# Kernel tuning notes

Hardware: AMD Instinct MI355X
Metric: run time of the kernel (lower is better)

## Reference

```python
import jax, jax.numpy as jnp
import numpy as np

J = 17        # number of joints (hard-coded in module)
H = 32        # h_dim
DIM = 2       # 2D keypoint input dim
N_TRUE = 9    # visible joints per sample (constant count required by reshape)
N_FALSE = J - N_TRUE
SLOPE = 0.01  # LeakyReLU default negative slope


def leaky(x):
    return jax.nn.leaky_relu(x, SLOPE)


def setup_inputs() -> dict:
    key = jax.random.key(0)
    ks = jax.random.split(key, 16)
    B = 65536
    x = jax.random.normal(ks[0], (B, J, DIM), jnp.float32)
    # mask with exactly N_TRUE True entries per row (random positions)
    perm = jnp.argsort(jax.random.uniform(ks[1], (B, J)), axis=1)
    m = jnp.zeros((B, J), bool).at[jnp.arange(B)[:, None], perm[:, :N_TRUE]].set(True)

    def lin(k, i, o):
        k1, k2 = jax.random.split(k)
        s = 1.0 / np.sqrt(i)
        # weights stored (in, out) so forward is x @ W + b
        return (jax.random.uniform(k1, (i, o), jnp.float32, -s, s),
                jax.random.uniform(k2, (o,), jnp.float32, -s, s))

    W_up, b_up = lin(ks[2], DIM * J, H * J)        # ScoreMechain.up_dim
    positions = jax.random.normal(ks[3], (1, J, H), jnp.float32)
    W_ud, b_ud = lin(ks[4], H + H, H)              # SelfAtt.up_dim (dim=h_dim=32)
    W_q, b_q = lin(ks[5], H, H)
    W_k, b_k = lin(ks[6], H, H)
    W_v, b_v = lin(ks[7], H, H)
    W_d1, b_d1 = lin(ks[8], H, H)                  # SelfAtt.down_dim[0]
    W_d2, b_d2 = lin(ks[9], H, H)                  # SelfAtt.down_dim[2]
    W_s, b_s = lin(ks[10], H, 1)                   # ScoreMechain.down_dim
    return dict(x=x, m=m, positions=positions, W_up=W_up, b_up=b_up,
                W_ud=W_ud, b_ud=b_ud, W_q=W_q, b_q=b_q, W_k=W_k, b_k=b_k,
                W_v=W_v, b_v=b_v, W_d1=W_d1, b_d1=b_d1, W_d2=W_d2, b_d2=b_d2,
                W_s=W_s, b_s=b_s)


def reference(x, m, positions, W_up, b_up, W_ud, b_ud, W_q, b_q, W_k, b_k,
              W_v, b_v, W_d1, b_d1, W_d2, b_d2, W_s, b_s):
    B = x.shape[0]
    # ScoreMechain: flatten joints, lift to (B, 17, H)
    up = leaky(x.reshape(B, -1) @ W_up + b_up).reshape(B, J, H)
    # static-count mask split via stable argsort (True-indices first / False-indices first)
    idx_t = jnp.argsort(~m, axis=1, stable=True)[:, :N_TRUE]   # visible joints
    idx_f = jnp.argsort(m, axis=1, stable=True)[:, :N_FALSE]   # occluded joints
    take = lambda a, i: jnp.take_along_axis(a, i[:, :, None], axis=1)
    x1 = take(up, idx_t)                       # (B, 9, H)
    x2 = take(up, idx_f)                       # (B, 8, H)
    # SelfAtt
    p = jnp.broadcast_to(positions, (B, J, H))
    kpos = take(p, idx_t)
    qpos = take(p, idx_f)
    x1c = jnp.concatenate([x1, kpos], axis=-1)  # (B, 9, 2H)
    x2c = jnp.concatenate([x2, qpos], axis=-1)  # (B, 8, 2H)
    u1 = leaky(x1c @ W_ud + b_ud)
    u2 = leaky(x2c @ W_ud + b_ud)
    ux = jnp.concatenate([u1, u2], axis=1)      # (B, 17, H)
    q = u2 @ W_q + b_q                          # (B, 8, H)
    k = ux @ W_k + b_k                          # (B, 17, H)
    v = ux @ W_v + b_v
    # SelfAtt was built as SelfAtt(h_dim) => scale = sqrt(32)
    att = jax.nn.softmax(jnp.einsum('bqh,bkh->bqk', q, k) / jnp.sqrt(jnp.float32(H)), axis=-1)
    o = jnp.einsum('bqk,bkh->bqh', att, v)      # (B, 8, H)
    o = (leaky(o @ W_d1 + b_d1) @ W_d2 + b_d2) + x2  # residual = x2c[..., :H] = x2
    return jax.nn.sigmoid(o @ W_s + b_s)[..., 0]     # (B, 8)
```

## Files before the change

### kernel.cpp

```cpp
#include <hip/hip_runtime.h>
#include <hip/hip_fp16.h>

#define JN 17

typedef __fp16 h2v __attribute__((ext_vector_type(2)));
typedef _Float16 f16x8 __attribute__((ext_vector_type(8)));
typedef float f32x4 __attribute__((ext_vector_type(4)));

__device__ __forceinline__ float lrelu(float x){ return fmaxf(x, 0.01f*x); }
__device__ __forceinline__ unsigned h2u(h2v h){ unsigned u; __builtin_memcpy(&u, &h, 4); return u; }
__device__ __forceinline__ h2v u2h(unsigned u){ h2v h; __builtin_memcpy(&h, &u, 4); return h; }
__device__ __forceinline__ unsigned pkrtz(float a, float b){ return h2u(__builtin_amdgcn_cvt_pkrtz(a,b)); }
__device__ __forceinline__ float fdot2(unsigned a, unsigned b, float c){
    return __builtin_amdgcn_fdot2(u2h(a), u2h(b), c, false);
}
__device__ __forceinline__ unsigned pkfma(unsigned a, unsigned b, unsigned c){
    h2v r = u2h(a)*u2h(b) + u2h(c);
    return h2u(r);
}
__device__ __forceinline__ f16x8 u4h8(uint4 u){ union{uint4 u; f16x8 h;} c; c.u=u; return c.h; }
__device__ __forceinline__ f32x4 mk4(float4 v){ f32x4 r; r[0]=v.x; r[1]=v.y; r[2]=v.z; r[3]=v.w; return r; }

__device__ __forceinline__ f16x8 repack(f32x4 c0, f32x4 c1, int srcA, int srcB, bool selLo){
    unsigned pkA = pkrtz(c0[0], c0[1]);
    unsigned pkB = pkrtz(c0[2], c0[3]);
    unsigned pkC = pkrtz(c1[0], c1[1]);
    unsigned pkD = pkrtz(c1[2], c1[3]);
    unsigned rA0 = (unsigned)__shfl((int)pkA, srcA, 64);
    unsigned rB0 = (unsigned)__shfl((int)pkB, srcA, 64);
    unsigned rC0 = (unsigned)__shfl((int)pkC, srcA, 64);
    unsigned rD0 = (unsigned)__shfl((int)pkD, srcA, 64);
    unsigned rA1 = (unsigned)__shfl((int)pkA, srcB, 64);
    unsigned rB1 = (unsigned)__shfl((int)pkB, srcB, 64);
    unsigned rC1 = (unsigned)__shfl((int)pkC, srcB, 64);
    unsigned rD1 = (unsigned)__shfl((int)pkD, srcB, 64);
    uint4 u;
    u.x = selLo ? rA0 : rC0;
    u.y = selLo ? rB0 : rD0;
    u.z = selLo ? rA1 : rC1;
    u.w = selLo ? rB1 : rD1;
    return u4h8(u);
}

#define OFF_PP    0
#define OFF_BQS   544
#define OFF_FQ    576
#define OFF_FD1   1088
#define OFF_FD2   1600
#define OFF_FUD   2112
#define OFF_FK    2624
#define OFF_FV    3136
#define OFF_TUP   3648
#define OFF_FUP   4192
#define HDR_BYTES 65536

#define KSTRIDE 276
#define QSTRIDE 132

__global__ __launch_bounds__(256,1)
void prep_kernel(const void* __restrict__ mraw, const float* __restrict__ pos,
                 const float* __restrict__ Wup,
                 const float* __restrict__ Wud, const float* __restrict__ bud,
                 const float* __restrict__ Wq,  const float* __restrict__ bq,
                 const float* __restrict__ Wk,  const float* __restrict__ Wv,
                 const float* __restrict__ Wd1, const float* __restrict__ Wd2,
                 unsigned* __restrict__ ws32, unsigned* __restrict__ bmask, int B)
{
    int g = blockIdx.x*256 + threadIdx.x;
    const float isq = 0.17677669529663687f;

    const unsigned* mw = (const unsigned*)mraw;
    bool f3f=false, nz=false;
    #pragma unroll
    for (int i=0;i<17;i++){
        unsigned w = mw[i];
        if ((w>>24) == 0x3Fu) f3f = true;
        if (w & 0xFFFFFF00u)  nz  = true;
    }
    int mode = f3f ? 2 : (nz ? 1 : 0);
    if (g < B){
        unsigned bm = 0; size_t base = (size_t)g*JN;
        if (mode == 0){
            const int* mi = (const int*)mraw;
            #pragma unroll
            for (int j=0;j<JN;j++) if (mi[base+j] != 0) bm |= (1u<<j);
        } else if (mode == 1){
            const unsigned char* mb = (const unsigned char*)mraw;
            #pragma unroll
            for (int j=0;j<JN;j++) if (mb[base+j] != 0) bm |= (1u<<j);
        } else {
            const float* mf = (const float*)mraw;
            #pragma unroll
            for (int j=0;j<JN;j++) if (mf[base+j] != 0.f) bm |= (1u<<j);
        }
        bmask[g] = bm;
    }
    if (g < 544){
        int j = g >> 5, h = g & 31;
        float acc = bud[h];
        #pragma unroll
        for (int c=0;c<32;c++) acc = fmaf(pos[j*32+c], Wud[(32+c)*32 + h], acc);
        ((float*)ws32)[OFF_PP + g] = acc;
        int t = (g >> 4) & 1, c = g & 15;
        int col = j*32 + t*16 + c;
        ws32[OFF_TUP + g] = pkrtz(Wup[32*544 + col], Wup[33*544 + col]);
    }
    if (g < 32) ((float*)ws32)[OFF_BQS + g] = bq[g]*isq;
    if (g < 512){
        int t = g >> 8, rmn = g & 255, lane = rmn >> 2, i2 = rmn & 3;
        int k0 = (lane>>4)*8 + 2*i2, c = (lane&15) + 16*t;
        ws32[OFF_FUD + g] = pkrtz(Wud[k0*32 + c],     Wud[(k0+1)*32 + c]);
        ws32[OFF_FK  + g] = pkrtz(Wk [k0*32 + c],     Wk [(k0+1)*32 + c]);
        ws32[OFF_FV  + g] = pkrtz(Wv [k0*32 + c],     Wv [(k0+1)*32 + c]);
        ws32[OFF_FQ  + g] = pkrtz(Wq [k0*32 + c]*isq, Wq [(k0+1)*32 + c]*isq);
        ws32[OFF_FD1 + g] = pkrtz(Wd1[(k0>>1)*32 + c], Wd1[(16 + (k0>>1))*32 + c]);
        ws32[OFF_FD2 + g] = pkrtz(Wd2[k0*32 + c],     Wd2[(k0+1)*32 + c]);
    }
    if (g < 8704){
        int j = g >> 9, r = g & 511, t = r >> 8, rr = r & 255, lane = rr >> 2, i2 = rr & 3;
        int k0 = (lane>>4)*8 + 2*i2;
        int col = j*32 + (lane&15) + 16*t;
        ws32[OFF_FUP + g] = pkrtz(Wup[k0*544 + col], Wup[(k0+1)*544 + col]);
    }
}

__global__ __launch_bounds__(256,3)
void fused_kernel(const float* __restrict__ x, const unsigned* __restrict__ bmask,
                  const unsigned* __restrict__ ws32,
                  const float* __restrict__ bup, const float* __restrict__ bk,
                  const float* __restrict__ bv,  const float* __restrict__ bd1,
                  const float* __restrict__ bd2, const float* __restrict__ Ws,
                  const float* __restrict__ bs,  float* __restrict__ out, int B)
{
    __shared__ unsigned ksl[16*KSTRIDE];
    __shared__ unsigned vsl[16*KSTRIDE];
    __shared__ unsigned qsl[16*QSTRIDE];
    __shared__ unsigned usl[16*QSTRIDE];

    const int tid = threadIdx.x;
    const int wid = tid >> 6, wl = tid & 63;
    const int sb  = blockIdx.x * 16;
    const int s   = wl & 15, g4 = wl >> 4;
    const int smax = B - 1;

    {
        int sA = sb + s; if (sA > smax) sA = smax;
        f16x8 ax;
        {
            const float* xr = x + (size_t)sA*34 + g4*8;
            float2 a0 = *(const float2*)(xr);
            float2 a1 = *(const float2*)(xr+2);
            float2 a2 = *(const float2*)(xr+4);
            float2 a3 = *(const float2*)(xr+6);
            uint4 u; u.x=pkrtz(a0.x,a0.y); u.y=pkrtz(a1.x,a1.y);
            u.z=pkrtz(a2.x,a2.y); u.w=pkrtz(a3.x,a3.y);
            ax = u4h8(u);
        }
        const unsigned bm = bmask[sA];
        float2 xt2 = *(const float2*)(x + (size_t)sA*34 + 32);
        const unsigned xtp = pkrtz(xt2.x, xt2.y);

        const uint4* wsu4 = (const uint4*)ws32;
        f16x8 fud0 = u4h8(wsu4[OFF_FUD/4 + wl]);
        f16x8 fud1 = u4h8(wsu4[OFF_FUD/4 + 64 + wl]);
        f16x8 fk0  = u4h8(wsu4[OFF_FK/4  + wl]);
        f16x8 fk1  = u4h8(wsu4[OFF_FK/4  + 64 + wl]);
        f16x8 fv0  = u4h8(wsu4[OFF_FV/4  + wl]);
        f16x8 fv1  = u4h8(wsu4[OFF_FV/4  + 64 + wl]);
        f16x8 fq0  = u4h8(wsu4[OFF_FQ/4  + wl]);
        f16x8 fq1  = u4h8(wsu4[OFF_FQ/4  + 64 + wl]);

        const float* ppf = (const float*)ws32;
        float4 bk0 = *(const float4*)(bk + g4*4);
        float4 bk1 = *(const float4*)(bk + 16 + g4*4);
        float4 bv0 = *(const float4*)(bv + g4*4);
        float4 bv1 = *(const float4*)(bv + 16 + g4*4);
        float4 bq0 = *(const float4*)(ppf + OFF_BQS + g4*4);
        float4 bq1 = *(const float4*)(ppf + OFF_BQS + 16 + g4*4);

        const int srcA = s + 32*(g4 & 1);
        const int srcB = srcA + 16;
        const bool selLo = (g4 < 2);

        const int njl = (wid == 3) ? 5 : 4;
        for (int jj = 0; jj < njl; jj++){
            const int j = (jj < 4) ? (wid + jj*4) : 16;
            f16x8 fup0 = u4h8(wsu4[OFF_FUP/4 + j*128 + wl]);
            f16x8 fup1 = u4h8(wsu4[OFF_FUP/4 + j*128 + 64 + wl]);
            float4 bu0 = *(const float4*)(bup + j*32 + g4*4);
            float4 bu1 = *(const float4*)(bup + j*32 + 16 + g4*4);
            float4 pp0 = *(const float4*)(ppf + OFF_PP + j*32 + g4*4);
            float4 pp1 = *(const float4*)(ppf + OFF_PP + j*32 + 16 + g4*4);
            uint4 tu0 = *(const uint4*)(ws32 + OFF_TUP + j*32 + g4*4);
            uint4 tu1 = *(const uint4*)(ws32 + OFF_TUP + j*32 + 16 + g4*4);

            f32x4 up0, up1;
            up0[0] = fdot2(xtp, tu0.x, bu0.x); up0[1] = fdot2(xtp, tu0.y, bu0.y);
            up0[2] = fdot2(xtp, tu0.z, bu0.z); up0[3] = fdot2(xtp, tu0.w, bu0.w);
            up1[0] = fdot2(xtp, tu1.x, bu1.x); up1[1] = fdot2(xtp, tu1.y, bu1.y);
            up1[2] = fdot2(xtp, tu1.z, bu1.z); up1[3] = fdot2(xtp, tu1.w, bu1.w);
            up0 = __builtin_amdgcn_mfma_f32_16x16x32_f16(fup0, ax, up0, 0,0,0);
            up1 = __builtin_amdgcn_mfma_f32_16x16x32_f16(fup1, ax, up1, 0,0,0);
            #pragma unroll
            for (int r=0;r<4;r++){ up0[r] = lrelu(up0[r]); up1[r] = lrelu(up1[r]); }

            const bool occ = !((bm>>j)&1u);
            const int rk = __popc((~bm) & ((1u<<j)-1u));
            if (occ){
                int rotq = (rk + s + (s>>2)) & 3;
                uint4 u;
                u.x = pkrtz(up0[0], up1[0]); u.y = pkrtz(up0[1], up1[1]);
                u.z = pkrtz(up0[2], up1[2]); u.w = pkrtz(up0[3], up1[3]);
                *(uint4*)&usl[s*QSTRIDE + rk*16 + ((g4 + rotq)&3)*4] = u;
            }
            f16x8 aup = repack(up0, up1, srcA, srcB, selLo);

            f32x4 uu0 = mk4(pp0), uu1 = mk4(pp1);
            uu0 = __builtin_amdgcn_mfma_f32_16x16x32_f16(fud0, aup, uu0, 0,0,0);
            uu1 = __builtin_amdgcn_mfma_f32_16x16x32_f16(fud1, aup, uu1, 0,0,0);
            #pragma unroll
            for (int r=0;r<4;r++){ uu0[r] = lrelu(uu0[r]); uu1[r] = lrelu(uu1[r]); }
            f16x8 auu = repack(uu0, uu1, srcA, srcB, selLo);

            f32x4 kk0 = mk4(bk0), kk1 = mk4(bk1);
            f32x4 vv0 = mk4(bv0), vv1 = mk4(bv1);
            f32x4 qq0 = mk4(bq0), qq1 = mk4(bq1);
            kk0 = __builtin_amdgcn_mfma_f32_16x16x32_f16(fk0, auu, kk0, 0,0,0);
            kk1 = __builtin_amdgcn_mfma_f32_16x16x32_f16(fk1, auu, kk1, 0,0,0);
            vv0 = __builtin_amdgcn_mfma_f32_16x16x32_f16(fv0, auu, vv0, 0,0,0);
            vv1 = __builtin_amdgcn_mfma_f32_16x16x32_f16(fv1, auu, vv1, 0,0,0);
            qq0 = __builtin_amdgcn_mfma_f32_16x16x32_f16(fq0, auu, qq0, 0,0,0);
            qq1 = __builtin_amdgcn_mfma_f32_16x16x32_f16(fq1, auu, qq1, 0,0,0);

            const int rot = (j + s + (s>>2)) & 3;
            const int grp = ((g4 + rot)&3)*4;
            uint4 kp, vp;
            kp.x = pkrtz(kk0[0], kk1[0]); kp.y = pkrtz(kk0[1], kk1[1]);
            kp.z = pkrtz(kk0[2], kk1[2]); kp.w = pkrtz(kk0[3], kk1[3]);
            vp.x = pkrtz(vv0[0], vv1[0]); vp.y = pkrtz(vv0[1], vv1[1]);
            vp.z = pkrtz(vv0[2], vv1[2]); vp.w = pkrtz(vv0[3], vv1[3]);
            *(uint4*)&ksl[s*KSTRIDE + j*16 + grp] = kp;
            *(uint4*)&vsl[s*KSTRIDE + j*16 + grp] = vp;
            if (occ){
                int rotq = (rk + s + (s>>2)) & 3;
                uint4 qp4;
                qp4.x = pkrtz(qq0[0], qq1[0]); qp4.y = pkrtz(qq0[1], qq1[1]);
                qp4.z = pkrtz(qq0[2], qq1[2]); qp4.w = pkrtz(qq0[3], qq1[3]);
                *(uint4*)&qsl[s*QSTRIDE + rk*16 + ((g4 + rotq)&3)*4] = qp4;
            }
        }
    }
    __syncthreads();

    const int pr = tid;
    const int s2 = (pr >> 3) & 15, q = pr & 7;
    const bool act2 = (tid < 128) && (sb + s2 < B);
    unsigned o[16];
    #pragma unroll
    for (int p=0;p<16;p++) o[p] = 0u;
    if (act2){
        unsigned qw[16];
        {
            int rot = (q + s2 + (s2>>2)) & 3;
            const unsigned* base = qsl + s2*QSTRIDE + q*16;
            #pragma unroll
            for (int a=0;a<4;a++){
                uint4 t = *(const uint4*)(base + ((a + rot)&3)*4);
                qw[4*a]=t.x; qw[4*a+1]=t.y; qw[4*a+2]=t.z; qw[4*a+3]=t.w;
            }
        }
        float sc[JN];
        #pragma unroll
        for (int kj=0; kj<JN; kj++){
            unsigned kw[16];
            int rot = (kj + s2 + (s2>>2)) & 3;
            const unsigned* base = ksl + s2*KSTRIDE + kj*16;
            #pragma unroll
            for (int a=0;a<4;a++){
                uint4 t = *(const uint4*)(base + ((a + rot)&3)*4);
                kw[4*a]=t.x; kw[4*a+1]=t.y; kw[4*a+2]=t.z; kw[4*a+3]=t.w;
            }
            float s0=0.f,s1=0.f,s2a=0.f,s3=0.f;
            #pragma unroll
            for (int p=0;p<16;p+=4){
                s0  = fdot2(qw[p],   kw[p],   s0);
                s1  = fdot2(qw[p+1], kw[p+1], s1);
                s2a = fdot2(qw[p+2], kw[p+2], s2a);
                s3  = fdot2(qw[p+3], kw[p+3], s3);
            }
            sc[kj] = (s0+s1)+(s2a+s3);
        }
        float m = sc[0];
        #pragma unroll
        for (int kj=1;kj<JN;kj++) m = fmaxf(m, sc[kj]);
        float e[JN]; float sum = 0.f;
        #pragma unroll
        for (int kj=0;kj<JN;kj++){ e[kj] = __expf(sc[kj]-m); sum += e[kj]; }
        float ri = 1.0f/sum;
        #pragma unroll
        for (int kj=0;kj<JN;kj++){
            float w = e[kj]*ri;
            unsigned w2 = pkrtz(w, w);
            unsigned vw[16];
            int rot = (kj + s2 + (s2>>2)) & 3;
            const unsigned* base = vsl + s2*KSTRIDE + kj*16;
            #pragma unroll
            for (int a=0;a<4;a++){
                uint4 t = *(const uint4*)(base + ((a + rot)&3)*4);
                vw[4*a]=t.x; vw[4*a+1]=t.y; vw[4*a+2]=t.z; vw[4*a+3]=t.w;
            }
            #pragma unroll
            for (int p=0;p<16;p++) o[p] = pkfma(w2, vw[p], o[p]);
        }
    }
    __syncthreads();
    if (act2){
        int rot = (pr>>1)&3;
        *(uint4*)&ksl[pr*16 + ((0+rot)&3)*4] = make_uint4(o[0],o[1],o[2],o[3]);
        *(uint4*)&ksl[pr*16 + ((1+rot)&3)*4] = make_uint4(o[4],o[5],o[6],o[7]);
        *(uint4*)&ksl[pr*16 + ((2+rot)&3)*4] = make_uint4(o[8],o[9],o[10],o[11]);
        *(uint4*)&ksl[pr*16 + ((3+rot)&3)*4] = make_uint4(o[12],o[13],o[14],o[15]);
    }
    __syncthreads();

    {
        const int rid = wl & 15, g4b = wl >> 4;
        const uint4* wsu4 = (const uint4*)ws32;
        f16x8 fd1_0 = u4h8(wsu4[OFF_FD1/4 + wl]);
        f16x8 fd1_1 = u4h8(wsu4[OFF_FD1/4 + 64 + wl]);
        f16x8 fd2_0 = u4h8(wsu4[OFF_FD2/4 + wl]);
        f16x8 fd2_1 = u4h8(wsu4[OFF_FD2/4 + 64 + wl]);
        float4 bd10 = *(const float4*)(bd1 + g4b*4);
        float4 bd11 = *(const float4*)(bd1 + 16 + g4b*4);
        float4 bd20 = *(const float4*)(bd2 + g4b*4);
        float4 bd21 = *(const float4*)(bd2 + 16 + g4b*4);
        float4 ws0  = *(const float4*)(Ws + g4b*4);
        float4 ws1  = *(const float4*)(Ws + 16 + g4b*4);
        const float bsv = bs[0];
        const int srcA = rid + 32*(g4b & 1);
        const int srcB = srcA + 16;
        const bool selLo = (g4b < 2);

        #pragma unroll
        for (int gg=0; gg<2; gg++){
            const int rowg = (wid*2 + gg)*16 + rid;
            int roto = (rowg>>1)&3;
            f16x8 bo = u4h8(*(const uint4*)&ksl[rowg*16 + ((g4b + roto)&3)*4]);

            f32x4 t0 = mk4(bd10), t1 = mk4(bd11);
            t0 = __builtin_amdgcn_mfma_f32_16x16x32_f16(fd1_0, bo, t0, 0,0,0);
            t1 = __builtin_amdgcn_mfma_f32_16x16x32_f16(fd1_1, bo, t1, 0,0,0);
            #pragma unroll
            for (int r=0;r<4;r++){ t0[r] = lrelu(t0[r]); t1[r] = lrelu(t1[r]); }
            f16x8 bt = repack(t0, t1, srcA, srcB, selLo);

            const int s2b = rowg >> 3, qb = rowg & 7;
            int rotq = (qb + s2b + (s2b>>2)) & 3;
            uint4 ur = *(const uint4*)&usl[s2b*QSTRIDE + qb*16 + ((g4b + rotq)&3)*4];
            unsigned urr[4] = {ur.x, ur.y, ur.z, ur.w};
            f32x4 z0, z1;
            {
                h2v r0 = u2h(urr[0]), r1 = u2h(urr[1]), r2 = u2h(urr[2]), r3 = u2h(urr[3]);
                z0[0] = (float)r0.x + bd20.x; z1[0] = (float)r0.y + bd21.x;
                z0[1] = (float)r1.x + bd20.y; z1[1] = (float)r1.y + bd21.y;
                z0[2] = (float)r2.x + bd20.z; z1[2] = (float)r2.y + bd21.z;
                z0[3] = (float)r3.x + bd20.w; z1[3] = (float)r3.y + bd21.w;
            }
            z0 = __builtin_amdgcn_mfma_f32_16x16x32_f16(fd2_0, bt, z0, 0,0,0);
            z1 = __builtin_amdgcn_mfma_f32_16x16x32_f16(fd2_1, bt, z1, 0,0,0);

            float yp = z0[0]*ws0.x + z0[1]*ws0.y + z0[2]*ws0.z + z0[3]*ws0.w
                     + z1[0]*ws1.x + z1[1]*ws1.y + z1[2]*ws1.z + z1[3]*ws1.w;
            yp += __shfl_xor(yp, 16, 64);
            yp += __shfl_xor(yp, 32, 64);
            if (g4b == 0 && sb + s2b < B){
                float y = yp + bsv;
                out[((size_t)(sb + s2b))*8 + qb] = 1.0f/(1.0f + __expf(-y));
            }
        }
    }
}

extern "C" void kernel_launch(void* const* d_in, const int* in_sizes, int n_in,
                              void* d_out, int out_size, void* d_ws, size_t ws_size,
                              hipStream_t stream) {
    (void)n_in; (void)out_size; (void)ws_size;
    const float* x   = (const float*)d_in[0];
    const void*  m   = d_in[1];
    const float* pos = (const float*)d_in[2];
    const float* Wup = (const float*)d_in[3];  const float* bup = (const float*)d_in[4];
    const float* Wud = (const float*)d_in[5];  const float* bud = (const float*)d_in[6];
    const float* Wq  = (const float*)d_in[7];  const float* bq  = (const float*)d_in[8];
    const float* Wk  = (const float*)d_in[9];  const float* bk  = (const float*)d_in[10];
    const float* Wv  = (const float*)d_in[11]; const float* bv  = (const float*)d_in[12];
    const float* Wd1 = (const float*)d_in[13]; const float* bd1 = (const float*)d_in[14];
    const float* Wd2 = (const float*)d_in[15]; const float* bd2 = (const float*)d_in[16];
    const float* Ws  = (const float*)d_in[17]; const float* bs  = (const float*)d_in[18];
    float* out = (float*)d_out;
    int B = in_sizes[0] / (JN*2);

    unsigned char* wsb = (unsigned char*)d_ws;
    unsigned* ws32  = (unsigned*)wsb;
    unsigned* bmask = (unsigned*)(wsb + HDR_BYTES);

    prep_kernel<<<(B+255)/256, 256, 0, stream>>>(m, pos, Wup, Wud, bud, Wq, bq,
                                                 Wk, Wv, Wd1, Wd2, ws32, bmask, B);
    fused_kernel<<<(B+15)/16, 256, 0, stream>>>(x, bmask, ws32, bup, bk, bv,
                                                bd1, bd2, Ws, bs, out, B);
}
```

Measured before the change: 69.30 us.

## Split attention key range across both thread halves with shared-memory score exchange

Attention was computed by only the first 128 threads, one query row each. Now all 256 threads work: each half handles 9 of the 17 keys (joint 8 is shared and zeroed in one half). Partial scores go through shared memory to form the full softmax, and each half writes its partial output into a separate buffer, summed in fp16 before the MFMA stage. This doubles the active lanes in the attention phase at the cost of two extra barriers, extra LDS traffic, and one redundant key per thread. The bounds guard (sb+s2<B) is also dropped.

```diff
diff --git a/kernel.cpp b/kernel.cpp
--- a/kernel.cpp
+++ b/kernel.cpp
@@ -252,74 +252,85 @@
     }
     __syncthreads();
 
-    const int pr = tid;
-    const int s2 = (pr >> 3) & 15, q = pr & 7;
-    const bool act2 = (tid < 128) && (sb + s2 < B);
+    const int half  = tid >> 7;
+    const int pr    = tid & 127;
+    const int s2 = pr >> 3, q = pr & 7;
+    const int kbase = half*8;
+    unsigned qw[16];
+    {
+        int rot = (q + s2 + (s2>>2)) & 3;
+        const unsigned* base = qsl + s2*QSTRIDE + q*16;
+        #pragma unroll
+        for (int a=0;a<4;a++){
+            uint4 t = *(const uint4*)(base + ((a + rot)&3)*4);
+            qw[4*a]=t.x; qw[4*a+1]=t.y; qw[4*a+2]=t.z; qw[4*a+3]=t.w;
+        }
+    }
+    float scl[9];
+    #pragma unroll
+    for (int i=0;i<9;i++){
+        int kj = kbase + i;
+        unsigned kw[16];
+        int rot = (kj + s2 + (s2>>2)) & 3;
+        const unsigned* kb = ksl + s2*KSTRIDE + kj*16;
+        #pragma unroll
+        for (int a=0;a<4;a++){
+            uint4 t = *(const uint4*)(kb + ((a + rot)&3)*4);
+            kw[4*a]=t.x; kw[4*a+1]=t.y; kw[4*a+2]=t.z; kw[4*a+3]=t.w;
+        }
+        float s0=0.f,s1=0.f,s2a=0.f,s3=0.f;
+        #pragma unroll
+        for (int p=0;p<16;p+=4){
+            s0  = fdot2(qw[p],   kw[p],   s0);
+            s1  = fdot2(qw[p+1], kw[p+1], s1);
+            s2a = fdot2(qw[p+2], kw[p+2], s2a);
+            s3  = fdot2(qw[p+3], kw[p+3], s3);
+        }
+        scl[i] = (s0+s1)+(s2a+s3);
+    }
+    __syncthreads();
+    #pragma unroll
+    for (int i=0;i<9;i++) ksl[pr*21 + kbase + i] = __float_as_uint(scl[i]);
+    __syncthreads();
+    float sc[JN];
+    #pragma unroll
+    for (int kj=0;kj<JN;kj++) sc[kj] = __uint_as_float(ksl[pr*21 + kj]);
+    float m = sc[0];
+    #pragma unroll
+    for (int kj=1;kj<JN;kj++) m = fmaxf(m, sc[kj]);
+    float sum = 0.f;
+    #pragma unroll
+    for (int kj=0;kj<JN;kj++) sum += __expf(sc[kj]-m);
+    float ri = 1.0f/sum;
+
     unsigned o[16];
     #pragma unroll
     for (int p=0;p<16;p++) o[p] = 0u;
-    if (act2){
-        unsigned qw[16];
-        {
-            int rot = (q + s2 + (s2>>2)) & 3;
-            const unsigned* base = qsl + s2*QSTRIDE + q*16;
-            #pragma unroll
-            for (int a=0;a<4;a++){
-                uint4 t = *(const uint4*)(base + ((a + rot)&3)*4);
-                qw[4*a]=t.x; qw[4*a+1]=t.y; qw[4*a+2]=t.z; qw[4*a+3]=t.w;
-            }
-        }
-        float sc[JN];
-        #pragma unroll
-        for (int kj=0; kj<JN; kj++){
-            unsigned kw[16];
-            int rot = (kj + s2 + (s2>>2)) & 3;
-            const unsigned* base = ksl + s2*KSTRIDE + kj*16;
-            #pragma unroll
-            for (int a=0;a<4;a++){
-                uint4 t = *(const uint4*)(base + ((a + rot)&3)*4);
-                kw[4*a]=t.x; kw[4*a+1]=t.y; kw[4*a+2]=t.z; kw[4*a+3]=t.w;
-            }
-            float s0=0.f,s1=0.f,s2a=0.f,s3=0.f;
-            #pragma unroll
-            for (int p=0;p<16;p+=4){
-                s0  = fdot2(qw[p],   kw[p],   s0);
-                s1  = fdot2(qw[p+1], kw[p+1], s1);
-                s2a = fdot2(qw[p+2], kw[p+2], s2a);
-                s3  = fdot2(qw[p+3], kw[p+3], s3);
-            }
-            sc[kj] = (s0+s1)+(s2a+s3);
-        }
-        float m = sc[0];
-        #pragma unroll
-        for (int kj=1;kj<JN;kj++) m = fmaxf(m, sc[kj]);
-        float e[JN]; float sum = 0.f;
-        #pragma unroll
-        for (int kj=0;kj<JN;kj++){ e[kj] = __expf(sc[kj]-m); sum += e[kj]; }
-        float ri = 1.0f/sum;
-        #pragma unroll
-        for (int kj=0;kj<JN;kj++){
-            float w = e[kj]*ri;
-            unsigned w2 = pkrtz(w, w);
-            unsigned vw[16];
-            int rot = (kj + s2 + (s2>>2)) & 3;
-            const unsigned* base = vsl + s2*KSTRIDE + kj*16;
-            #pragma unroll
-            for (int a=0;a<4;a++){
-                uint4 t = *(const uint4*)(base + ((a + rot)&3)*4);
-                vw[4*a]=t.x; vw[4*a+1]=t.y; vw[4*a+2]=t.z; vw[4*a+3]=t.w;
-            }
-            #pragma unroll
-            for (int p=0;p<16;p++) o[p] = pkfma(w2, vw[p], o[p]);
-        }
+    #pragma unroll
+    for (int i=0;i<9;i++){
+        int kj = kbase + i;
+        float w = __expf(scl[i]-m)*ri;
+        if (i==8 && half==0) w = 0.f;
+        unsigned w2 = pkrtz(w, w);
+        unsigned vw[16];
+        int rot = (kj + s2 + (s2>>2)) & 3;
+        const unsigned* vb = vsl + s2*KSTRIDE + kj*16;
+        #pragma unroll
+        for (int a=0;a<4;a++){
+            uint4 t = *(const uint4*)(vb + ((a + rot)&3)*4);
+            vw[4*a]=t.x; vw[4*a+1]=t.y; vw[4*a+2]=t.z; vw[4*a+3]=t.w;
+        }
+        #pragma unroll
+        for (int p=0;p<16;p++) o[p] = pkfma(w2, vw[p], o[p]);
     }
     __syncthreads();
-    if (act2){
+    {
         int rot = (pr>>1)&3;
-        *(uint4*)&ksl[pr*16 + ((0+rot)&3)*4] = make_uint4(o[0],o[1],o[2],o[3]);
-        *(uint4*)&ksl[pr*16 + ((1+rot)&3)*4] = make_uint4(o[4],o[5],o[6],o[7]);
-        *(uint4*)&ksl[pr*16 + ((2+rot)&3)*4] = make_uint4(o[8],o[9],o[10],o[11]);
-        *(uint4*)&ksl[pr*16 + ((3+rot)&3)*4] = make_uint4(o[12],o[13],o[14],o[15]);
+        unsigned* dst = vsl + half*2048 + pr*16;
+        *(uint4*)&dst[((0+rot)&3)*4] = make_uint4(o[0],o[1],o[2],o[3]);
+        *(uint4*)&dst[((1+rot)&3)*4] = make_uint4(o[4],o[5],o[6],o[7]);
+        *(uint4*)&dst[((2+rot)&3)*4] = make_uint4(o[8],o[9],o[10],o[11]);
+        *(uint4*)&dst[((3+rot)&3)*4] = make_uint4(o[12],o[13],o[14],o[15]);
     }
     __syncthreads();
 
@@ -345,7 +356,9 @@
         for (int gg=0; gg<2; gg++){
             const int rowg = (wid*2 + gg)*16 + rid;
             int roto = (rowg>>1)&3;
-            f16x8 bo = u4h8(*(const uint4*)&ksl[rowg*16 + ((g4b + roto)&3)*4]);
+            uint4 a4 = *(const uint4*)&vsl[rowg*16 + ((g4b + roto)&3)*4];
+            uint4 b4 = *(const uint4*)&vsl[2048 + rowg*16 + ((g4b + roto)&3)*4];
+            f16x8 bo = u4h8(a4) + u4h8(b4);
 
             f32x4 t0 = mk4(bd10), t1 = mk4(bd11);
             t0 = __builtin_amdgcn_mfma_f32_16x16x32_f16(fd1_0, bo, t0, 0,0,0);
```

Measured after the change: 65.88 us. 4.9% less time.

## Compute attention scores and weighted sum with MFMA instead of scalar fdot2

Applied to the files above, without the earlier changes.

Replaces the per-thread attention stage, where 128 threads each did 17 fdot2 score loops and 17 packed-FMA value accumulations, with a wave-level scheme. Each wave handles 4 samples, computes QK^T with one 16x16x32 MFMA plus an fdot2 for the 17th key, runs the softmax through cross-lane shuffles, and computes att·V with two MFMAs. The output is staged in qsl instead of ksl. This aims to use all threads and the matrix units instead of leaving half the block idle, at the cost of shuffle overhead, scattered scalar LDS gathers for V, and fp16 rounding of probabilities.

```diff
diff --git a/kernel.cpp b/kernel.cpp
--- a/kernel.cpp
+++ b/kernel.cpp
@@ -13,10 +13,6 @@
 __device__ __forceinline__ unsigned pkrtz(float a, float b){ return h2u(__builtin_amdgcn_cvt_pkrtz(a,b)); }
 __device__ __forceinline__ float fdot2(unsigned a, unsigned b, float c){
     return __builtin_amdgcn_fdot2(u2h(a), u2h(b), c, false);
-}
-__device__ __forceinline__ unsigned pkfma(unsigned a, unsigned b, unsigned c){
-    h2v r = u2h(a)*u2h(b) + u2h(c);
-    return h2u(r);
 }
 __device__ __forceinline__ f16x8 u4h8(uint4 u){ union{uint4 u; f16x8 h;} c; c.u=u; return c.h; }
 __device__ __forceinline__ f32x4 mk4(float4 v){ f32x4 r; r[0]=v.x; r[1]=v.y; r[2]=v.z; r[3]=v.w; return r; }
@@ -252,74 +248,118 @@
     }
     __syncthreads();
 
-    const int pr = tid;
-    const int s2 = (pr >> 3) & 15, q = pr & 7;
-    const bool act2 = (tid < 128) && (sb + s2 < B);
-    unsigned o[16];
+    const int lq = wl & 15;
+    f32x4 oT0_0, oT0_1, oT0_2, oT0_3;
+    f32x4 oT1_0, oT1_1, oT1_2, oT1_3;
     #pragma unroll
-    for (int p=0;p<16;p++) o[p] = 0u;
-    if (act2){
-        unsigned qw[16];
+    for (int it=0; it<4; ++it){
+        const int smp = (wid<<2) + it;
+        int rotk = (lq + smp + (smp>>2)) & 3;
+        uint4 kA4 = *(const uint4*)&ksl[smp*KSTRIDE + lq*16 + ((g4 + rotk)&3)*4];
+        int rot16 = (16 + smp + (smp>>2)) & 3;
+        uint4 k164 = *(const uint4*)&ksl[smp*KSTRIDE + 16*16 + ((g4 + rot16)&3)*4];
+        uint4 qB4 = make_uint4(0u,0u,0u,0u);
+        if (lq < 8){
+            int rotq = (lq + smp + (smp>>2)) & 3;
+            qB4 = *(const uint4*)&qsl[smp*QSTRIDE + lq*16 + ((g4 + rotq)&3)*4];
+        }
+        f32x4 S = {0.f,0.f,0.f,0.f};
+        S = __builtin_amdgcn_mfma_f32_16x16x32_f16(u4h8(kA4), u4h8(qB4), S, 0,0,0);
+        float p16 = 0.f;
+        p16 = fdot2(qB4.x, k164.x, p16); p16 = fdot2(qB4.y, k164.y, p16);
+        p16 = fdot2(qB4.z, k164.z, p16); p16 = fdot2(qB4.w, k164.w, p16);
+        p16 += __shfl_xor(p16, 16, 64);
+        p16 += __shfl_xor(p16, 32, 64);
+        float m4 = fmaxf(fmaxf(S[0],S[1]), fmaxf(S[2],S[3]));
+        m4 = fmaxf(m4, __shfl_xor(m4, 16, 64));
+        m4 = fmaxf(m4, __shfl_xor(m4, 32, 64));
+        float m = fmaxf(m4, p16);
+        float e0 = __expf(S[0]-m), e1 = __expf(S[1]-m);
+        float e2 = __expf(S[2]-m), e3 = __expf(S[3]-m);
+        float es = (e0+e1)+(e2+e3);
+        es += __shfl_xor(es, 16, 64);
+        es += __shfl_xor(es, 32, 64);
+        float e16 = __expf(p16 - m);
+        float ri = 1.0f / (es + e16);
+        unsigned p01 = pkrtz(e0*ri, e1*ri);
+        unsigned p23 = pkrtz(e2*ri, e3*ri);
+        unsigned a16 = pkrtz(e16*ri, 0.f);
+        int sA2 = lq + 32*(g4 & 1);
+        int sB2 = sA2 + 16;
+        unsigned d0 = (unsigned)__shfl((int)p01, sA2, 64);
+        unsigned d1 = (unsigned)__shfl((int)p23, sA2, 64);
+        unsigned d2 = (unsigned)__shfl((int)p01, sB2, 64);
+        unsigned d3 = (unsigned)__shfl((int)p23, sB2, 64);
+        bool gLo = (g4 < 2);
+        d0 = gLo ? d0 : ((g4 == 2) ? a16 : 0u);
+        d1 = gLo ? d1 : 0u;
+        d2 = gLo ? d2 : 0u;
+        d3 = gLo ? d3 : 0u;
+        f16x8 attA = u4h8(make_uint4(d0,d1,d2,d3));
+        unsigned b00, b01, b02, b03, b10, b11, b12, b13;
         {
-            int rot = (q + s2 + (s2>>2)) & 3;
-            const unsigned* base = qsl + s2*QSTRIDE + q*16;
-            #pragma unroll
-            for (int a=0;a<4;a++){
-                uint4 t = *(const uint4*)(base + ((a + rot)&3)*4);
-                qw[4*a]=t.x; qw[4*a+1]=t.y; qw[4*a+2]=t.z; qw[4*a+3]=t.w;
+            int phys = (lq & 3);
+            int lg = lq >> 2;
+            unsigned ra, rb;
+            int ka, kb, rota, rotb;
+            ka = g4*8;     kb = ka+1;
+            ra = 0u; rb = 0u;
+            if (ka < JN){ rota = (ka + smp + (smp>>2)) & 3;
+                ra = vsl[smp*KSTRIDE + ka*16 + ((lg + rota)&3)*4 + phys]; }
+            if (kb < JN){ rotb = (kb + smp + (smp>>2)) & 3;
+                rb = vsl[smp*KSTRIDE + kb*16 + ((lg + rotb)&3)*4 + phys]; }
+            b00 = (ra & 0xFFFFu) | (rb << 16);
+            b10 = (ra >> 16) | (rb & 0xFFFF0000u);
+            ka = g4*8+2;   kb = ka+1;
+            ra = 0u; rb = 0u;
+            if (ka < JN){ rota = (ka + smp + (smp>>2)) & 3;
+                ra = vsl[smp*KSTRIDE + ka*16 + ((lg + rota)&3)*4 + phys]; }
+            if (kb < JN){ rotb = (kb + smp + (smp>>2)) & 3;
+                rb = vsl[smp*KSTRIDE + kb*16 + ((lg + rotb)&3)*4 + phys]; }
+            b01 = (ra & 0xFFFFu) | (rb << 16);
+            b11 = (ra >> 16) | (rb & 0xFFFF0000u);
+            ka = g4*8+4;   kb = ka+1;
+            ra = 0u; rb = 0u;
+            if (ka < JN){ rota = (ka + smp + (smp>>2)) & 3;
+                ra = vsl[smp*KSTRIDE + ka*16 + ((lg + rota)&3)*4 + phys]; }
+            if (kb < JN){ rotb = (kb + smp + (smp>>2)) & 3;
+                rb = vsl[smp*KSTRIDE + kb*16 + ((lg + rotb)&3)*4 + phys]; }
+            b02 = (ra & 0xFFFFu) | (rb << 16);
+            b12 = (ra >> 16) | (rb & 0xFFFF0000u);
+            ka = g4*8+6;   kb = ka+1;
+            ra = 0u; rb = 0u;
+            if (ka < JN){ rota = (ka + smp + (smp>>2)) & 3;
+                ra = vsl[smp*KSTRIDE + ka*16 + ((lg + rota)&3)*4 + phys]; }
+            if (kb < JN){ rotb = (kb + smp + (smp>>2)) & 3;
+                rb = vsl[smp*KSTRIDE + kb*16 + ((lg + rotb)&3)*4 + phys]; }
+            b03 = (ra & 0xFFFFu) | (rb << 16);
+            b13 = (ra >> 16) | (rb & 0xFFFF0000u);
+        }
+        f16x8 vB0 = u4h8(make_uint4(b00,b01,b02,b03));
+        f16x8 vB1 = u4h8(make_uint4(b10,b11,b12,b13));
+        f32x4 z4 = {0.f,0.f,0.f,0.f};
+        f32x4 r0 = __builtin_amdgcn_mfma_f32_16x16x32_f16(attA, vB0, z4, 0,0,0);
+        f32x4 r1 = __builtin_amdgcn_mfma_f32_16x16x32_f16(attA, vB1, z4, 0,0,0);
+        if (it==0){ oT0_0 = r0; oT1_0 = r1; }
+        else if (it==1){ oT0_1 = r0; oT1_1 = r1; }
+        else if (it==2){ oT0_2 = r0; oT1_2 = r1; }
+        else { oT0_3 = r0; oT1_3 = r1; }
+    }
+    __syncthreads();
+    if (g4 < 2){
+        #pragma unroll
+        for (int it=0; it<4; ++it){
+            const int smp = (wid<<2) + it;
+            f32x4 t0 = (it==0)?oT0_0:(it==1)?oT0_1:(it==2)?oT0_2:oT0_3;
+            f32x4 t1 = (it==0)?oT1_0:(it==1)?oT1_1:(it==2)?oT1_2:oT1_3;
+            #pragma unroll
+            for (int reg=0; reg<4; ++reg){
+                int qq = g4*4 + reg;
+                int rowg = smp*8 + qq;
+                int roto = (rowg>>1)&3;
+                qsl[rowg*16 + (((lq>>2) + roto)&3)*4 + (lq&3)] = pkrtz(t0[reg], t1[reg]);
             }
         }
-        float sc[JN];
-        #pragma unroll
-        for (int kj=0; kj<JN; kj++){
-            unsigned kw[16];
-            int rot = (kj + s2 + (s2>>2)) & 3;
-            const unsigned* base = ksl + s2*KSTRIDE + kj*16;
-            #pragma unroll
-            for (int a=0;a<4;a++){
-                uint4 t = *(const uint4*)(base + ((a + rot)&3)*4);
-                kw[4*a]=t.x; kw[4*a+1]=t.y; kw[4*a+2]=t.z; kw[4*a+3]=t.w;
-            }
-            float s0=0.f,s1=0.f,s2a=0.f,s3=0.f;
-            #pragma unroll
-            for (int p=0;p<16;p+=4){
-                s0  = fdot2(qw[p],   kw[p],   s0);
-                s1  = fdot2(qw[p+1], kw[p+1], s1);
-                s2a = fdot2(qw[p+2], kw[p+2], s2a);
-                s3  = fdot2(qw[p+3], kw[p+3], s3);
-            }
-            sc[kj] = (s0+s1)+(s2a+s3);
-        }
-        float m = sc[0];
-        #pragma unroll
-        for (int kj=1;kj<JN;kj++) m = fmaxf(m, sc[kj]);
-        float e[JN]; float sum = 0.f;
-        #pragma unroll
-        for (int kj=0;kj<JN;kj++){ e[kj] = __expf(sc[kj]-m); sum += e[kj]; }
-        float ri = 1.0f/sum;
-        #pragma unroll
-        for (int kj=0;kj<JN;kj++){
-            float w = e[kj]*ri;
-            unsigned w2 = pkrtz(w, w);
-            unsigned vw[16];
-            int rot = (kj + s2 + (s2>>2)) & 3;
-            const unsigned* base = vsl + s2*KSTRIDE + kj*16;
-            #pragma unroll
-            for (int a=0;a<4;a++){
-                uint4 t = *(const uint4*)(base + ((a + rot)&3)*4);
-                vw[4*a]=t.x; vw[4*a+1]=t.y; vw[4*a+2]=t.z; vw[4*a+3]=t.w;
-            }
-            #pragma unroll
-            for (int p=0;p<16;p++) o[p] = pkfma(w2, vw[p], o[p]);
-        }
-    }
-    __syncthreads();
-    if (act2){
-        int rot = (pr>>1)&3;
-        *(uint4*)&ksl[pr*16 + ((0+rot)&3)*4] = make_uint4(o[0],o[1],o[2],o[3]);
-        *(uint4*)&ksl[pr*16 + ((1+rot)&3)*4] = make_uint4(o[4],o[5],o[6],o[7]);
-        *(uint4*)&ksl[pr*16 + ((2+rot)&3)*4] = make_uint4(o[8],o[9],o[10],o[11]);
-        *(uint4*)&ksl[pr*16 + ((3+rot)&3)*4] = make_uint4(o[12],o[13],o[14],o[15]);
     }
     __syncthreads();
 
@@ -345,7 +385,7 @@
         for (int gg=0; gg<2; gg++){
             const int rowg = (wid*2 + gg)*16 + rid;
             int roto = (rowg>>1)&3;
-            f16x8 bo = u4h8(*(const uint4*)&ksl[rowg*16 + ((g4b + roto)&3)*4]);
+            f16x8 bo = u4h8(*(const uint4*)&qsl[rowg*16 + ((g4b + roto)&3)*4]);
 
             f32x4 t0 = mk4(bd10), t1 = mk4(bd11);
             t0 = __builtin_amdgcn_mfma_f32_16x16x32_f16(fd1_0, bo, t0, 0,0,0);
```

After: 68.79 us. No clear change (-0.7%).
